# Kernel tuning notes

Hardware: AMD Instinct MI355X
Metric: run time of the kernel (lower is better)

Reference implementation:

```python
import jax, jax.numpy as jnp
import numpy as np

N_BLADES = 32  # Cl(4,1) has 2^5 = 32 basis blades


def _gp_sign_bitwise(a, b):
    """Sign of e_a * e_b in Cl(4,1) via bitwise swap counting (numpy, static)."""
    a = np.asarray(a, dtype=np.int64)
    b = np.asarray(b, dtype=np.int64)
    a, b = np.broadcast_arrays(a, b)
    swaps = np.zeros(a.shape, dtype=np.int64)
    for i in range(5):
        b_has_i = (b >> i) & 1
        mask_gt = (~((1 << (i + 1)) - 1)) & 31
        val = a & mask_gt
        pc = (val & 1) + ((val >> 1) & 1) + ((val >> 2) & 1) + ((val >> 3) & 1) + ((val >> 4) & 1)
        swaps += b_has_i * pc
    comm_sign = np.where(swaps % 2 == 0, 1.0, -1.0)
    metric_sign = np.where(((a & 16) & (b & 16)) > 0, -1.0, 1.0)
    return (comm_sign * metric_sign).astype(np.float32)


_M = np.arange(N_BLADES)
PERM = (_M[:, None] ^ _M[None, :]).astype(np.int32)        # PERM[k, m] = m ^ k
SIGNS = _gp_sign_bitwise(_M[None, :], PERM)                 # sign(m, m^k), [32, 32]
PERM_J = jnp.asarray(PERM)
SIGNS_J = jnp.asarray(SIGNS)


def setup_inputs() -> dict:
    key = jax.random.key(0)
    kx, kw = jax.random.split(key)
    B, In, Out = 1024, 256, 256
    x = jax.random.normal(kx, (B, In, N_BLADES), dtype=jnp.float32)
    std = 0.5 / (In * N_BLADES) ** 0.5
    weight = jax.random.normal(kw, (Out, In, N_BLADES), dtype=jnp.float32) * std
    return {"x": x, "weight": weight}


def reference(x, weight):
    # x: [B, In, 32], weight: [Out, In, 32]
    # out[b, o, k] = sum_{i, m} x[b, i, m^k] * sign(m, m^k) * w[o, i, m]
    x_g = x[..., PERM_J] * SIGNS_J                 # [B, In, 32(k), 32(m)]
    out = jnp.einsum('bikm,oim->bok', x_g, weight)  # [B, Out, 32]
    return out
```

## Files before the change

### kernel.cpp

```cpp
#include <hip/hip_runtime.h>

typedef __attribute__((ext_vector_type(8))) short bf16x8;
typedef __attribute__((ext_vector_type(16))) float f32x16;
typedef __attribute__((ext_vector_type(8))) unsigned short ushort8;

#define N_BLADES 32
#define B_DIM 1024
#define IN_DIM 256
#define OUT_DIM 256
#define K_DIM (IN_DIM * N_BLADES)
#define N_DIM (OUT_DIM * N_BLADES)


__device__ __forceinline__ unsigned short f2bf(float f) {
    unsigned int u = __float_as_uint(f);
    u = (u + 0x7fff + ((u >> 16) & 1)) >> 16;
    return (unsigned short)u;
}

__device__ __forceinline__ float gp_sign(int a, int b) {
    int swaps = 0;
#pragma unroll
    for (int i = 0; i < 5; ++i) {
        int mask = (~((1 << (i + 1)) - 1)) & 31;
        swaps += ((b >> i) & 1) * __popc(a & mask);
    }
    float s = (swaps & 1) ? -1.0f : 1.0f;
    if (a & b & 16) s = -s;
    return s;
}

__device__ __forceinline__ void gload_lds16(const void* g, void* l) {
    __builtin_amdgcn_global_load_lds(
        (const __attribute__((address_space(1))) unsigned int*)g,
        (__attribute__((address_space(3))) unsigned int*)l, 16, 0, 0);
}

#define FENCE() asm volatile("" ::: "memory")
#define BAR()    { FENCE(); __builtin_amdgcn_s_barrier(); FENCE(); }
#define SCHED0() __builtin_amdgcn_sched_barrier(0)
#define LGKM(n)  { asm volatile("s_waitcnt lgkmcnt(" #n ")" ::: "memory"); }
#define VMC(n)   { asm volatile("s_waitcnt vmcnt(" #n ")" ::: "memory"); }

__global__ __launch_bounds__(256) void cast_x2_kernel(const float* __restrict__ x,
                                                      unsigned short* __restrict__ xb2) {
    int t = blockIdx.x * 256 + threadIdx.x;
    int o  = t & 7;
    int b  = (t >> 3) & 1023;
    int kt = t >> 13;
    const float4* src = (const float4*)(x + (long)b * K_DIM + kt * 64 + o * 8);
    float4 a = src[0], c = src[1];
    ushort8 pk;
    pk[0] = f2bf(a.x); pk[1] = f2bf(a.y); pk[2] = f2bf(a.z); pk[3] = f2bf(a.w);
    pk[4] = f2bf(c.x); pk[5] = f2bf(c.y); pk[6] = f2bf(c.z); pk[7] = f2bf(c.w);
    *(ushort8*)(xb2 + ((size_t)kt * 8192 + b * 8 + o) * 8) = pk;
}

__global__ __launch_bounds__(256) void cast_w_perm_kernel(const float* __restrict__ w,
                                                          unsigned short* __restrict__ wb2) {
    int t = blockIdx.x * 256 + threadIdx.x;
    int o31   = t & 31;
    int c16   = (t >> 5) & 7;
    int panel = (t >> 8) & 7;
    int kt    = t >> 11;
    int o  = panel * 32 + o31;
    int k0 = kt * 64 + c16 * 8;
    const float4* src = (const float4*)(w + (long)o * K_DIM + k0);
    float4 a = src[0], b = src[1];
    ushort8 pk;
    pk[0] = f2bf(a.x); pk[1] = f2bf(a.y); pk[2] = f2bf(a.z); pk[3] = f2bf(a.w);
    pk[4] = f2bf(b.x); pk[5] = f2bf(b.y); pk[6] = f2bf(b.z); pk[7] = f2bf(b.w);
    *(ushort8*)(wb2 + (size_t)t * 8) = pk;
}

__device__ __forceinline__ bf16x8 shuffle_sign(bf16x8 v, int jx,
                                               unsigned int m0, unsigned int m1,
                                               unsigned int m2, unsigned int m3) {
    union { bf16x8 v8; unsigned int w[4]; } a, b;
    a.v8 = v;
    int s = jx >> 1;
    unsigned int t0 = (s & 1) ? a.w[1] : a.w[0];
    unsigned int t1 = (s & 1) ? a.w[0] : a.w[1];
    unsigned int t2 = (s & 1) ? a.w[3] : a.w[2];
    unsigned int t3 = (s & 1) ? a.w[2] : a.w[3];
    unsigned int u0 = (s & 2) ? t2 : t0;
    unsigned int u1 = (s & 2) ? t3 : t1;
    unsigned int u2 = (s & 2) ? t0 : t2;
    unsigned int u3 = (s & 2) ? t1 : t3;
    if (jx & 1) {
        u0 = (u0 >> 16) | (u0 << 16);
        u1 = (u1 >> 16) | (u1 << 16);
        u2 = (u2 >> 16) | (u2 << 16);
        u3 = (u3 >> 16) | (u3 << 16);
    }
    b.w[0] = u0 ^ m0; b.w[1] = u1 ^ m1; b.w[2] = u2 ^ m2; b.w[3] = u3 ^ m3;
    return b.v8;
}


__global__ __launch_bounds__(512, 1) void gemm_big_kernel(const unsigned short* __restrict__ xb2,
                                                          const unsigned short* __restrict__ wb2,
                                                          float* __restrict__ C0,
                                                          float* __restrict__ C1) {
    __shared__ char lds[163840];

    const int tid  = threadIdx.x;
    const int lane = tid & 63;
    const int wid  = tid >> 6;
    const int wr   = wid >> 2;
    const int wc   = wid & 3;
    const int l31  = lane & 31;
    const int l5   = lane >> 5;

    const int  kblk = blockIdx.x;
    const int  mb   = blockIdx.y;
    const int  z    = blockIdx.z;
    float* __restrict__ C = z ? C1 : C0;
    const int  kt0  = z * 64;
    const int  jx   = kblk & 7;
    const int  kq   = (kblk >> 3) & 3;

    const int rA = tid >> 1;
    const int g4 = (tid & 1) * 4;
    const char* xbB = (const char*)xb2 + (long)(mb * 256 + rA) * 128;
    const int o0 = ((g4 + 0) ^ kq) * 16;
    const int o1 = ((g4 + 1) ^ kq) * 16;
    const int o2 = ((g4 + 2) ^ kq) * 16;
    const int o3 = ((g4 + 3) ^ kq) * 16;
    const int adw_base = (rA >> 5) * 4096 + (rA & 31) * 16;
    const int adw0 = adw_base + (g4 + 0) * 512;
    const int adw1 = adw_base + (g4 + 1) * 512;
    const int adw2 = adw_base + (g4 + 2) * 512;
    const int adw3 = adw_base + (g4 + 3) * 512;

    unsigned int mk[4][4];
#pragma unroll
    for (int q = 0; q < 4; ++q)
#pragma unroll
        for (int w_ = 0; w_ < 4; ++w_) {
            unsigned int m_ = 0;
#pragma unroll
            for (int e2 = 0; e2 < 2; ++e2) {
                int m = 8 * q + 2 * w_ + e2;
                if (gp_sign(m, m ^ kblk) < 0.0f) m_ |= 0x8000u << (16 * e2);
            }
            mk[q][w_] = m_;
        }

    const int  tid16 = tid * 16;
    const char* bSrc = (const char*)wb2 + tid16;
    const int aPan = wr * 16384;
    const int bPan = 65536 + wc * 8192;
    const int cc0 = (0 + l5) * 512 + l31 * 16;
    const int cc1 = (2 + l5) * 512 + l31 * 16;
    const int cc2 = (4 + l5) * 512 + l31 * 16;
    const int cc3 = (6 + l5) * 512 + l31 * 16;

#define B_STAGE(br, ktv) { \
    const long tb_ = (long)(ktv) * 32768; \
    _Pragma("unroll") for (int n = 0; n < 4; ++n) \
        gload_lds16(bSrc + tb_ + n * 8192, lds + 65536 + (br) * 32768 + n * 8192 + tid16); }
#define A_LOAD(S, ktv) { \
    const char* p_ = xbB + (long)(ktv) * 131072; \
    S##0 = *(const bf16x8*)(p_ + o0); \
    S##1 = *(const bf16x8*)(p_ + o1); \
    S##2 = *(const bf16x8*)(p_ + o2); \
    S##3 = *(const bf16x8*)(p_ + o3); }
#define A_SHUF_WRITE(S, ab) { \
    bf16x8 f0_ = shuffle_sign(S##0, jx, mk[0][0], mk[0][1], mk[0][2], mk[0][3]); \
    bf16x8 f1_ = shuffle_sign(S##1, jx, mk[1][0], mk[1][1], mk[1][2], mk[1][3]); \
    bf16x8 f2_ = shuffle_sign(S##2, jx, mk[2][0], mk[2][1], mk[2][2], mk[2][3]); \
    bf16x8 f3_ = shuffle_sign(S##3, jx, mk[3][0], mk[3][1], mk[3][2], mk[3][3]); \
    *(bf16x8*)(lds + (ab) * 32768 + adw0) = f0_; \
    *(bf16x8*)(lds + (ab) * 32768 + adw1) = f1_; \
    *(bf16x8*)(lds + (ab) * 32768 + adw2) = f2_; \
    *(bf16x8*)(lds + (ab) * 32768 + adw3) = f3_; }
#define READ_B01(br) { \
    _Pragma("unroll") for (int nt = 0; nt < 2; ++nt) { \
        bF[nt][0] = *(const bf16x8*)(lds + bPan + (br)*32768 + nt*4096 + cc0); \
        bF[nt][1] = *(const bf16x8*)(lds + bPan + (br)*32768 + nt*4096 + cc1); } }
#define READ_B23(br) { \
    _Pragma("unroll") for (int nt = 0; nt < 2; ++nt) { \
        bF[nt][2] = *(const bf16x8*)(lds + bPan + (br)*32768 + nt*4096 + cc2); \
        bF[nt][3] = *(const bf16x8*)(lds + bPan + (br)*32768 + nt*4096 + cc3); } }
#define READ_A01(ab) { \
    _Pragma("unroll") for (int mt = 0; mt < 4; ++mt) { \
        aF[mt][0] = *(const bf16x8*)(lds + (ab)*32768 + aPan + mt*4096 + cc0); \
        aF[mt][1] = *(const bf16x8*)(lds + (ab)*32768 + aPan + mt*4096 + cc1); } }
#define READ_A23(ab) { \
    _Pragma("unroll") for (int mt = 0; mt < 4; ++mt) { \
        aF[mt][0] = *(const bf16x8*)(lds + (ab)*32768 + aPan + mt*4096 + cc2); \
        aF[mt][1] = *(const bf16x8*)(lds + (ab)*32768 + aPan + mt*4096 + cc3); } }
#define MFG01() \
    _Pragma("unroll") for (int s = 0; s < 2; ++s) \
    _Pragma("unroll") for (int mt = 0; mt < 4; ++mt) \
    _Pragma("unroll") for (int nt = 0; nt < 2; ++nt) \
        acc[mt][nt] = __builtin_amdgcn_mfma_f32_32x32x16_bf16(aF[mt][s], bF[nt][s], acc[mt][nt], 0, 0, 0);
#define MFG23() \
    _Pragma("unroll") for (int s = 0; s < 2; ++s) \
    _Pragma("unroll") for (int mt = 0; mt < 4; ++mt) \
    _Pragma("unroll") for (int nt = 0; nt < 2; ++nt) \
        acc[mt][nt] = __builtin_amdgcn_mfma_f32_32x32x16_bf16(aF[mt][s], bF[nt][2 + s], acc[mt][nt], 0, 0, 0);

    f32x16 acc[4][2];
#pragma unroll
    for (int mt = 0; mt < 4; ++mt)
#pragma unroll
        for (int nt = 0; nt < 2; ++nt) acc[mt][nt] = (f32x16)0.0f;

    bf16x8 aE0, aE1, aE2, aE3, aO0, aO1, aO2, aO3;
    bf16x8 aF[4][2], bF[2][4];

    A_LOAD(aE, kt0);
    SCHED0();
    VMC(0);
    A_SHUF_WRITE(aE, 0);
    SCHED0();
    B_STAGE(0, kt0);
    SCHED0();
    A_LOAD(aO, kt0 + 1);
    SCHED0();
    B_STAGE(1, kt0 + 1);
    SCHED0();
    LGKM(0);
    BAR();

#define TILE(Jv, ABR, ABW, SW, SL, BRR, BRS) { \
    const int ktp = (kt0 + (Jv) + 2) & 127; \
    VMC(4);                     \
    A_SHUF_WRITE(SW, ABW);      \
    SCHED0(); \
    READ_B01(BRR); \
    READ_A01(ABR); \
    READ_B23(BRR);              \
    SCHED0(); \
    A_LOAD(SL, ktp);            \
    SCHED0(); \
    B_STAGE(BRS, ktp);          \
    SCHED0(); \
    LGKM(4);                    \
    MFG01(); \
    READ_A23(ABR); \
    SCHED0(); \
    LGKM(0); \
    MFG23(); \
    BAR(); }

    for (int t = 0; t < 60; t += 6) {
        TILE(t + 0, 0, 1, aO, aE, 0, 2);
        TILE(t + 1, 1, 0, aE, aO, 1, 0);
        TILE(t + 2, 0, 1, aO, aE, 2, 1);
        TILE(t + 3, 1, 0, aE, aO, 0, 2);
        TILE(t + 4, 0, 1, aO, aE, 1, 0);
        TILE(t + 5, 1, 0, aE, aO, 2, 1);
    }
    TILE(60, 0, 1, aO, aE, 0, 2);
    TILE(61, 1, 0, aE, aO, 1, 0);
    TILE(62, 0, 1, aO, aE, 2, 1);
    TILE(63, 1, 0, aE, aO, 0, 2);

#pragma unroll
    for (int mt = 0; mt < 4; ++mt)
#pragma unroll
        for (int nt = 0; nt < 2; ++nt) {
            long c = (long)kblk * 256 + wc * 64 + nt * 32 + l31;
#pragma unroll
            for (int r = 0; r < 16; ++r) {
                int  rl = (r & 3) + 8 * (r >> 2) + 4 * l5;
                long rb = (long)mb * 256 + wr * 128 + mt * 32 + rl;
                C[rb * N_DIM + c] = acc[mt][nt][r];
            }
        }

#undef B_STAGE
#undef A_LOAD
#undef A_SHUF_WRITE
#undef READ_B01
#undef READ_B23
#undef READ_A01
#undef READ_A23
#undef MFG01
#undef MFG23
#undef TILE
}

__global__ __launch_bounds__(256) void transpose_add_kernel(const float* __restrict__ C0,
                                                            const float* __restrict__ C1,
                                                            float* __restrict__ out) {
    __shared__ float t[32 * 260];
    const int tid = threadIdx.x;
    const long b  = blockIdx.x;
    const float4* s0 = (const float4*)(C0 + b * N_DIM);
    const float4* s1 = (const float4*)(C1 + b * N_DIM);
    float4*       dst = (float4*)(out + b * N_DIM);
#pragma unroll
    for (int r = 0; r < 8; ++r) {
        int f = tid + r * 256;
        float4 v = s0[f], u = s1[f];
        v.x += u.x; v.y += u.y; v.z += u.z; v.w += u.w;
        int k  = f >> 6;
        int c4 = (f & 63) * 4;
        *(float4*)&t[k * 260 + c4] = v;
    }
    __syncthreads();
#pragma unroll
    for (int r = 0; r < 8; ++r) {
        int g  = tid + r * 256;
        int o  = g >> 3;
        int k0 = (g & 7) * 4;
        float4 v;
        v.x = t[(k0 + 0) * 260 + o];
        v.y = t[(k0 + 1) * 260 + o];
        v.z = t[(k0 + 2) * 260 + o];
        v.w = t[(k0 + 3) * 260 + o];
        dst[g] = v;
    }
}

__global__ __launch_bounds__(256) void fallback_gp_kernel(const float* __restrict__ x,
                                                          const float* __restrict__ w,
                                                          float* __restrict__ out) {
    __shared__ float xs[IN_DIM * 32];
    __shared__ float tab[1024];
    int tid = threadIdx.x;
    for (int idx = tid; idx < 1024; idx += 256) {
        int m = idx >> 5, k = idx & 31;
        tab[idx] = gp_sign(m, m ^ k);
    }
    int b = blockIdx.x;
    const float4* xrow = (const float4*)(x + (long)b * K_DIM);
    float4* xs4 = (float4*)xs;
    for (int idx = tid; idx < 2048; idx += 256) xs4[idx] = xrow[idx];
    __syncthreads();

    int wid = tid >> 6, lane = tid & 63;
    int o = blockIdx.y * 8 + wid;
    int k = lane & 31, half = lane >> 5;
    float acc = 0.f;
    const float* wrow = w + (long)o * K_DIM + half * 4096;
    for (int i = 0; i < 128; ++i) {
        int ib = (half * 128 + i) * 32;
#pragma unroll
        for (int m = 0; m < 32; ++m) {
            acc += xs[ib + (m ^ k)] * tab[m * 32 + k] * wrow[i * 32 + m];
        }
    }
    acc += __shfl_down(acc, 32);
    if (half == 0) out[((long)b * OUT_DIM + o) * 32 + k] = acc;
}

extern "C" void kernel_launch(void* const* d_in, const int* in_sizes, int n_in,
                              void* d_out, int out_size, void* d_ws, size_t ws_size,
                              hipStream_t stream) {
    const float* x = (const float*)d_in[0];
    const float* w = (const float*)d_in[1];
    float* out = (float*)d_out;

    const size_t xb_bytes = (size_t)B_DIM * K_DIM * 2;
    const size_t wb_bytes = (size_t)OUT_DIM * IN_DIM * 32 * 2;
    const size_t cw_bytes = (size_t)B_DIM * N_DIM * 4;
    const size_t need = xb_bytes + wb_bytes + 2 * cw_bytes;

    if (ws_size >= need) {
        unsigned short* xbp = (unsigned short*)d_ws;
        unsigned short* wbp = (unsigned short*)((char*)d_ws + xb_bytes);
        float* c0 = (float*)((char*)d_ws + xb_bytes + wb_bytes);
        float* c1 = (float*)((char*)d_ws + xb_bytes + wb_bytes + cw_bytes);

        cast_x2_kernel<<<dim3(4096), dim3(256), 0, stream>>>(x, xbp);
        cast_w_perm_kernel<<<dim3(1024), dim3(256), 0, stream>>>(w, wbp);
        gemm_big_kernel<<<dim3(32, 4, 2), dim3(512), 0, stream>>>(xbp, wbp, c0, c1);
        transpose_add_kernel<<<dim3(B_DIM), dim3(256), 0, stream>>>(c0, c1, out);
    } else {
        fallback_gp_kernel<<<dim3(B_DIM, OUT_DIM / 8), dim3(256), 0, stream>>>(x, w, out);
    }
}
```

Measured before the change: 189.9 us.

## Swizzle A LDS layout, split MFMA into four phases, collapse A staging registers

Applies an XOR swizzle to the A-tile LDS write and read addresses to reduce bank conflicts. The MFMA loop is restructured into four k-phases that alternate X/Y fragment registers, with finer LGKM waits so LDS reads overlap MFMAs. The even/odd A staging registers are merged into one set to cut register pressure, and the launch attribute is changed to amdgpu_waves_per_eu(2,2). The risks are a register-allocation change that could spill, and swizzle correctness, since read and write must use matching XOR patterns.

```diff
diff --git a/kernel.cpp b/kernel.cpp
--- a/kernel.cpp
+++ b/kernel.cpp
@@ -98,10 +98,12 @@
 }
 
 
-__global__ __launch_bounds__(512, 1) void gemm_big_kernel(const unsigned short* __restrict__ xb2,
-                                                          const unsigned short* __restrict__ wb2,
-                                                          float* __restrict__ C0,
-                                                          float* __restrict__ C1) {
+__global__ __launch_bounds__(512)
+__attribute__((amdgpu_waves_per_eu(2, 2)))
+void gemm_big_kernel(const unsigned short* __restrict__ xb2,
+                     const unsigned short* __restrict__ wb2,
+                     float* __restrict__ C0,
+                     float* __restrict__ C1) {
     __shared__ char lds[163840];
 
     const int tid  = threadIdx.x;
@@ -127,7 +129,8 @@
     const int o1 = ((g4 + 1) ^ kq) * 16;
     const int o2 = ((g4 + 2) ^ kq) * 16;
     const int o3 = ((g4 + 3) ^ kq) * 16;
-    const int adw_base = (rA >> 5) * 4096 + (rA & 31) * 16;
+    const int apos = ((rA & 31) ^ g4) * 16;
+    const int adw_base = (rA >> 5) * 4096 + apos;
     const int adw0 = adw_base + (g4 + 0) * 512;
     const int adw1 = adw_base + (g4 + 1) * 512;
     const int adw2 = adw_base + (g4 + 2) * 512;
@@ -151,56 +154,38 @@
     const char* bSrc = (const char*)wb2 + tid16;
     const int aPan = wr * 16384;
     const int bPan = 65536 + wc * 8192;
-    const int cc0 = (0 + l5) * 512 + l31 * 16;
-    const int cc1 = (2 + l5) * 512 + l31 * 16;
-    const int cc2 = (4 + l5) * 512 + l31 * 16;
-    const int cc3 = (6 + l5) * 512 + l31 * 16;
 
 #define B_STAGE(br, ktv) { \
     const long tb_ = (long)(ktv) * 32768; \
     _Pragma("unroll") for (int n = 0; n < 4; ++n) \
         gload_lds16(bSrc + tb_ + n * 8192, lds + 65536 + (br) * 32768 + n * 8192 + tid16); }
-#define A_LOAD(S, ktv) { \
+#define A_LOAD(ktv) { \
     const char* p_ = xbB + (long)(ktv) * 131072; \
-    S##0 = *(const bf16x8*)(p_ + o0); \
-    S##1 = *(const bf16x8*)(p_ + o1); \
-    S##2 = *(const bf16x8*)(p_ + o2); \
-    S##3 = *(const bf16x8*)(p_ + o3); }
-#define A_SHUF_WRITE(S, ab) { \
-    bf16x8 f0_ = shuffle_sign(S##0, jx, mk[0][0], mk[0][1], mk[0][2], mk[0][3]); \
-    bf16x8 f1_ = shuffle_sign(S##1, jx, mk[1][0], mk[1][1], mk[1][2], mk[1][3]); \
-    bf16x8 f2_ = shuffle_sign(S##2, jx, mk[2][0], mk[2][1], mk[2][2], mk[2][3]); \
-    bf16x8 f3_ = shuffle_sign(S##3, jx, mk[3][0], mk[3][1], mk[3][2], mk[3][3]); \
+    S0 = *(const bf16x8*)(p_ + o0); \
+    S1 = *(const bf16x8*)(p_ + o1); \
+    S2 = *(const bf16x8*)(p_ + o2); \
+    S3 = *(const bf16x8*)(p_ + o3); }
+#define A_SHUF_WRITE(ab) { \
+    bf16x8 f0_ = shuffle_sign(S0, jx, mk[0][0], mk[0][1], mk[0][2], mk[0][3]); \
+    bf16x8 f1_ = shuffle_sign(S1, jx, mk[1][0], mk[1][1], mk[1][2], mk[1][3]); \
+    bf16x8 f2_ = shuffle_sign(S2, jx, mk[2][0], mk[2][1], mk[2][2], mk[2][3]); \
+    bf16x8 f3_ = shuffle_sign(S3, jx, mk[3][0], mk[3][1], mk[3][2], mk[3][3]); \
     *(bf16x8*)(lds + (ab) * 32768 + adw0) = f0_; \
     *(bf16x8*)(lds + (ab) * 32768 + adw1) = f1_; \
     *(bf16x8*)(lds + (ab) * 32768 + adw2) = f2_; \
     *(bf16x8*)(lds + (ab) * 32768 + adw3) = f3_; }
-#define READ_B01(br) { \
-    _Pragma("unroll") for (int nt = 0; nt < 2; ++nt) { \
-        bF[nt][0] = *(const bf16x8*)(lds + bPan + (br)*32768 + nt*4096 + cc0); \
-        bF[nt][1] = *(const bf16x8*)(lds + bPan + (br)*32768 + nt*4096 + cc1); } }
-#define READ_B23(br) { \
-    _Pragma("unroll") for (int nt = 0; nt < 2; ++nt) { \
-        bF[nt][2] = *(const bf16x8*)(lds + bPan + (br)*32768 + nt*4096 + cc2); \
-        bF[nt][3] = *(const bf16x8*)(lds + bPan + (br)*32768 + nt*4096 + cc3); } }
-#define READ_A01(ab) { \
-    _Pragma("unroll") for (int mt = 0; mt < 4; ++mt) { \
-        aF[mt][0] = *(const bf16x8*)(lds + (ab)*32768 + aPan + mt*4096 + cc0); \
-        aF[mt][1] = *(const bf16x8*)(lds + (ab)*32768 + aPan + mt*4096 + cc1); } }
-#define READ_A23(ab) { \
-    _Pragma("unroll") for (int mt = 0; mt < 4; ++mt) { \
-        aF[mt][0] = *(const bf16x8*)(lds + (ab)*32768 + aPan + mt*4096 + cc2); \
-        aF[mt][1] = *(const bf16x8*)(lds + (ab)*32768 + aPan + mt*4096 + cc3); } }
-#define MFG01() \
-    _Pragma("unroll") for (int s = 0; s < 2; ++s) \
+#define READ_A(AR, ab, p, xr) { \
+    _Pragma("unroll") for (int mt = 0; mt < 4; ++mt) \
+        AR[mt] = *(const bf16x8*)(lds + (ab)*32768 + aPan + mt*4096 \
+                                  + (2*(p) + l5)*512 + ((l31 ^ (xr))*16)); }
+#define READ_B(br, p) { \
+    _Pragma("unroll") for (int nt = 0; nt < 2; ++nt) \
+        bF[nt][p] = *(const bf16x8*)(lds + bPan + (br)*32768 + nt*4096 \
+                                     + (2*(p) + l5)*512 + l31*16); }
+#define MFG(AR, p) \
     _Pragma("unroll") for (int mt = 0; mt < 4; ++mt) \
     _Pragma("unroll") for (int nt = 0; nt < 2; ++nt) \
-        acc[mt][nt] = __builtin_amdgcn_mfma_f32_32x32x16_bf16(aF[mt][s], bF[nt][s], acc[mt][nt], 0, 0, 0);
-#define MFG23() \
-    _Pragma("unroll") for (int s = 0; s < 2; ++s) \
-    _Pragma("unroll") for (int mt = 0; mt < 4; ++mt) \
-    _Pragma("unroll") for (int nt = 0; nt < 2; ++nt) \
-        acc[mt][nt] = __builtin_amdgcn_mfma_f32_32x32x16_bf16(aF[mt][s], bF[nt][2 + s], acc[mt][nt], 0, 0, 0);
+        acc[mt][nt] = __builtin_amdgcn_mfma_f32_32x32x16_bf16(AR[mt], bF[nt][p], acc[mt][nt], 0, 0, 0);
 
     f32x16 acc[4][2];
 #pragma unroll
@@ -208,56 +193,60 @@
 #pragma unroll
         for (int nt = 0; nt < 2; ++nt) acc[mt][nt] = (f32x16)0.0f;
 
-    bf16x8 aE0, aE1, aE2, aE3, aO0, aO1, aO2, aO3;
-    bf16x8 aF[4][2], bF[2][4];
-
-    A_LOAD(aE, kt0);
+    bf16x8 S0, S1, S2, S3;
+    bf16x8 X[4], Y[4];
+    bf16x8 bF[2][4];
+
+    A_LOAD(kt0);
     SCHED0();
     VMC(0);
-    A_SHUF_WRITE(aE, 0);
+    A_SHUF_WRITE(0);
     SCHED0();
     B_STAGE(0, kt0);
     SCHED0();
-    A_LOAD(aO, kt0 + 1);
+    A_LOAD(kt0 + 1);
     SCHED0();
     B_STAGE(1, kt0 + 1);
     SCHED0();
     LGKM(0);
     BAR();
 
-#define TILE(Jv, ABR, ABW, SW, SL, BRR, BRS) { \
+#define TILE(Jv, AB, ABW, BRR, BRS) { \
     const int ktp = (kt0 + (Jv) + 2) & 127; \
     VMC(4);                     \
-    A_SHUF_WRITE(SW, ABW);      \
-    SCHED0(); \
-    READ_B01(BRR); \
-    READ_A01(ABR); \
-    READ_B23(BRR);              \
-    SCHED0(); \
-    A_LOAD(SL, ktp);            \
+    A_SHUF_WRITE(ABW);          \
+    SCHED0(); \
+    READ_B(BRR, 0); READ_B(BRR, 1); \
+    READ_A(X, AB, 0, 0); \
+    READ_A(Y, AB, 1, 0);        \
+    SCHED0(); \
+    A_LOAD(ktp);                \
     SCHED0(); \
     B_STAGE(BRS, ktp);          \
     SCHED0(); \
-    LGKM(4);                    \
-    MFG01(); \
-    READ_A23(ABR); \
-    SCHED0(); \
-    LGKM(0); \
-    MFG23(); \
+    LGKM(4);  MFG(X, 0);        \
+    READ_B(BRR, 2); READ_B(BRR, 3); \
+    READ_A(X, AB, 2, 4);        \
+    SCHED0(); \
+    LGKM(8);  MFG(Y, 1);        \
+    READ_A(Y, AB, 3, 4);        \
+    SCHED0(); \
+    LGKM(4);  MFG(X, 2);        \
+    LGKM(0);  MFG(Y, 3); \
     BAR(); }
 
     for (int t = 0; t < 60; t += 6) {
-        TILE(t + 0, 0, 1, aO, aE, 0, 2);
-        TILE(t + 1, 1, 0, aE, aO, 1, 0);
-        TILE(t + 2, 0, 1, aO, aE, 2, 1);
-        TILE(t + 3, 1, 0, aE, aO, 0, 2);
-        TILE(t + 4, 0, 1, aO, aE, 1, 0);
-        TILE(t + 5, 1, 0, aE, aO, 2, 1);
-    }
-    TILE(60, 0, 1, aO, aE, 0, 2);
-    TILE(61, 1, 0, aE, aO, 1, 0);
-    TILE(62, 0, 1, aO, aE, 2, 1);
-    TILE(63, 1, 0, aE, aO, 0, 2);
+        TILE(t + 0, 0, 1, 0, 2);
+        TILE(t + 1, 1, 0, 1, 0);
+        TILE(t + 2, 0, 1, 2, 1);
+        TILE(t + 3, 1, 0, 0, 2);
+        TILE(t + 4, 0, 1, 1, 0);
+        TILE(t + 5, 1, 0, 2, 1);
+    }
+    TILE(60, 0, 1, 0, 2);
+    TILE(61, 1, 0, 1, 0);
+    TILE(62, 0, 1, 2, 1);
+    TILE(63, 1, 0, 0, 2);
 
 #pragma unroll
     for (int mt = 0; mt < 4; ++mt)
@@ -275,12 +264,9 @@
 #undef B_STAGE
 #undef A_LOAD
 #undef A_SHUF_WRITE
-#undef READ_B01
-#undef READ_B23
-#undef READ_A01
-#undef READ_A23
-#undef MFG01
-#undef MFG23
+#undef READ_A
+#undef READ_B
+#undef MFG
 #undef TILE
 }
 
```

Result: faster. 157.8 us (-16.9%).
